# Kernel optimization log

Hardware: AMD Instinct MI355X
Metric: run time of the kernel (lower is better)

Reference implementation:

```python
import jax, jax.numpy as jnp
import numpy as np

B, T, D = 8, 4096, 512
EXPAND = 2
DI = D * EXPAND          # d_inner = 1024
K = 7                    # d_conv
LN_EPS = 1e-5


def setup_inputs() -> dict:
    key = jax.random.key(0)
    ks = jax.random.split(key, 12)
    s = 0.02
    return {
        "x": jax.random.normal(ks[0], (B, T, D), dtype=jnp.float32),
        # shared input projection (no bias): weight (2*DI, D), torch Linear layout
        "in_proj_w": jax.random.normal(ks[1], (2 * DI, D), dtype=jnp.float32) * s,
        # forward Conv1DSequenceMixer: depthwise conv (DI,1,K) + bias, proj Linear (DI,DI)+bias
        "conv_fwd_w": jax.random.normal(ks[2], (DI, 1, K), dtype=jnp.float32) * s,
        "conv_fwd_b": jnp.zeros((DI,), dtype=jnp.float32),
        "proj_fwd_w": jax.random.normal(ks[3], (DI, DI), dtype=jnp.float32) * s,
        "proj_fwd_b": jnp.zeros((DI,), dtype=jnp.float32),
        # backward Conv1DSequenceMixer
        "conv_bwd_w": jax.random.normal(ks[4], (DI, 1, K), dtype=jnp.float32) * s,
        "conv_bwd_b": jnp.zeros((DI,), dtype=jnp.float32),
        "proj_bwd_w": jax.random.normal(ks[5], (DI, DI), dtype=jnp.float32) * s,
        "proj_bwd_b": jnp.zeros((DI,), dtype=jnp.float32),
        # diagonal term and gate scale
        "diag_weight": jnp.full((DI,), 0.1, dtype=jnp.float32),
        "gate_scale": jnp.full((1,), 0.5, dtype=jnp.float32),
        # output projection (no bias): (D, DI)
        "out_proj_w": jax.random.normal(ks[6], (D, DI), dtype=jnp.float32) * s,
        # LayerNorm
        "ln_g": jnp.ones((D,), dtype=jnp.float32),
        "ln_b": jnp.zeros((D,), dtype=jnp.float32),
    }


def _seq_mixer(x, conv_w, conv_b, proj_w, proj_b):
    """Conv1DSequenceMixer: causal depthwise conv + SiLU(Linear). x: (B,T,C)."""
    C = x.shape[-1]
    # torch pads both sides by K-1 then truncates to T -> equivalent to causal left-pad
    xp = jnp.pad(x, ((0, 0), (K - 1, 0), (0, 0)))            # (B, T+K-1, C)
    y = jax.lax.conv_general_dilated(
        xp.transpose(0, 2, 1), conv_w, window_strides=(1,), padding="VALID",
        dimension_numbers=("NCH", "OIH", "NCH"), feature_group_count=C,
    )                                                         # (B, C, T)
    y = y.transpose(0, 2, 1) + conv_b                         # (B, T, C)
    y = jnp.einsum("btc,oc->bto", y, proj_w) + proj_b
    return jax.nn.silu(y)


def _shift_right(x):
    """Shift one step right along time, zero-padding the first step."""
    return jnp.pad(x, ((0, 0), (1, 0), (0, 0)))[:, :-1, :]


def reference(x, in_proj_w, conv_fwd_w, conv_fwd_b, proj_fwd_w, proj_fwd_b,
              conv_bwd_w, conv_bwd_b, proj_bwd_w, proj_bwd_b,
              diag_weight, gate_scale, out_proj_w, ln_g, ln_b):
    residual = x
    xz = jnp.einsum("btd,ed->bte", x, in_proj_w)              # (B,T,2*DI)
    x_proj, z = xz[..., :DI], xz[..., DI:]

    y_fwd = _shift_right(_seq_mixer(x_proj, conv_fwd_w, conv_fwd_b, proj_fwd_w, proj_fwd_b))

    x_flip = jnp.flip(x_proj, axis=1)
    y_bwd = _shift_right(_seq_mixer(x_flip, conv_bwd_w, conv_bwd_b, proj_bwd_w, proj_bwd_b))
    y_bwd = jnp.flip(y_bwd, axis=1)

    y = y_fwd + y_bwd + x_proj * diag_weight                  # quasiseparable sum
    y = y * jax.nn.silu(z) * gate_scale                       # SiLU gate + scale
    y = jnp.einsum("bte,de->btd", y, out_proj_w)              # out_proj (no bias)

    h = residual + y                                          # dropout=0 (eval)
    mu = jnp.mean(h, axis=-1, keepdims=True)
    var = jnp.var(h, axis=-1, keepdims=True)
    return (h - mu) * jax.lax.rsqrt(var + LN_EPS) * ln_g + ln_b
```

## Files before the change

kernel.cpp:

```cpp
#include <hip/hip_runtime.h>
#include <hip/hip_bf16.h>
#include <cstdint>

#define T_SEQ  4096
#define DMODEL 512
#define DINNER 1024
#define MTOT   32768

typedef __bf16 bf16_t;
typedef bf16_t bf16x8 __attribute__((ext_vector_type(8)));
typedef bf16_t bf16x4v __attribute__((ext_vector_type(4)));
typedef float  f32x4  __attribute__((ext_vector_type(4)));

__device__ __forceinline__ void async_copy16(const bf16_t* g, bf16_t* l) {
  __builtin_amdgcn_global_load_lds(
      (const __attribute__((address_space(1))) void*)g,
      (__attribute__((address_space(3))) void*)l,
      16, 0, 0);
}

__device__ __forceinline__ float silu_f(float v) {
  return v / (1.f + __expf(-v));
}

__device__ __forceinline__ int xcd_swizzle_flat() {
  const int nwg = gridDim.x * gridDim.y;
  const int orig = blockIdx.y * gridDim.x + blockIdx.x;
  const int q = nwg >> 3, r = nwg & 7;
  const int xcd = orig & 7, lid = orig >> 3;
  return (xcd < r ? xcd * (q + 1) : r * (q + 1) + (xcd - r) * q) + lid;
}

__global__ __launch_bounds__(256) void cast_kernel(
    const float* __restrict__ s, bf16_t* __restrict__ d, int n4)
{
  const int i = blockIdx.x * 256 + threadIdx.x;
  if (i < n4) {
    const f32x4 v = ((const f32x4*)s)[i];
    bf16x4v o;
    o[0] = (bf16_t)v[0]; o[1] = (bf16_t)v[1];
    o[2] = (bf16_t)v[2]; o[3] = (bf16_t)v[3];
    ((bf16x4v*)d)[i] = o;
  }
}

__global__ __launch_bounds__(256) void wtr_kernel(
    const float* __restrict__ w, float* __restrict__ wt)
{
  const int i = blockIdx.x * 256 + threadIdx.x;
  if (i < 7 * DINNER) {
    const int c = i & (DINNER - 1);
    const int k = i >> 10;
    wt[i] = w[c * 7 + k];
  }
}

template <int EPI>
__global__ __launch_bounds__(256, 2) void gemm_bt(
    const bf16_t* __restrict__ A, const bf16_t* __restrict__ B,
    bf16_t* __restrict__ Cb, float* __restrict__ Cf,
    const float* __restrict__ resid,
    int N, int K)
{
  constexpr int BM = 128, BN = 128, BK = 64;
  __shared__ __attribute__((aligned(16))) bf16_t sA0[BM * BK];
  __shared__ __attribute__((aligned(16))) bf16_t sB0[BN * BK];
  __shared__ __attribute__((aligned(16))) bf16_t sA1[BM * BK];
  __shared__ __attribute__((aligned(16))) bf16_t sB1[BN * BK];

  const int tid  = threadIdx.x;
  const int bflat = xcd_swizzle_flat();
  const int m0 = (bflat / gridDim.x) * BM;
  const int n0 = (bflat % gridDim.x) * BN;

  const int w    = tid >> 6, lane = tid & 63;
  const int wm   = (w & 1) << 6, wn = (w >> 1) << 6;
  const int quad = lane >> 4, lrow = lane & 15;

  const int f0 = tid << 3;
  const int sr = f0 >> 6, sc = f0 & 63;

  f32x4 acc[4][4] = {};

  auto STAGE = [&](int kt, bf16_t* dA, bf16_t* dB) {
#pragma unroll
    for (int i = 0; i < 4; ++i) {
      const int f = f0 + (i << 11);
      const int r = sr + (i << 5);
      async_copy16(&A[(size_t)(m0 + r) * K + kt + sc], &dA[f]);
      async_copy16(&B[(size_t)(n0 + r) * K + kt + sc], &dB[f]);
    }
  };

  auto COMPUTE = [&](const bf16_t* cA, const bf16_t* cB) {
#pragma unroll
    for (int ks = 0; ks < 2; ++ks) {
      const int ko = ks * 32 + (quad << 3);
      bf16x8 av[4], bv[4];
#pragma unroll
      for (int i = 0; i < 4; ++i) {
        av[i] = *(const bf16x8*)&cA[(wm + i * 16 + lrow) * BK + ko];
        bv[i] = *(const bf16x8*)&cB[(wn + i * 16 + lrow) * BK + ko];
      }
#pragma unroll
      for (int mi = 0; mi < 4; ++mi)
#pragma unroll
        for (int ni = 0; ni < 4; ++ni)
          acc[mi][ni] = __builtin_amdgcn_mfma_f32_16x16x32_bf16(
              av[mi], bv[ni], acc[mi][ni], 0, 0, 0);
    }
  };

  STAGE(0, sA0, sB0);
  __syncthreads();

  for (int kt = 0; kt < K; kt += 2 * BK) {
    if (kt + BK < K) STAGE(kt + BK, sA1, sB1);
    COMPUTE(sA0, sB0);
    __syncthreads();
    if (kt + 2 * BK < K) STAGE(kt + 2 * BK, sA0, sB0);
    COMPUTE(sA1, sB1);
    __syncthreads();
  }

#pragma unroll
  for (int mi = 0; mi < 4; ++mi)
#pragma unroll
    for (int ni = 0; ni < 4; ++ni)
#pragma unroll
      for (int r = 0; r < 4; ++r) {
        const int row = m0 + wm + mi * 16 + (quad << 2) + r;
        const int col = n0 + wn + ni * 16 + lrow;
        float v = acc[mi][ni][r];
        if constexpr (EPI == 0) {
          Cb[(size_t)row * N + col] = (bf16_t)v;
        } else {
          v += resid[(size_t)row * N + col];
          Cf[(size_t)row * N + col] = v;
        }
      }
}

__global__ __launch_bounds__(256, 2) void gemm_dual(
    const bf16_t* __restrict__ A1, const bf16_t* __restrict__ A2,
    const bf16_t* __restrict__ B1, const bf16_t* __restrict__ B2,
    const float* __restrict__ b1, const float* __restrict__ b2,
    const bf16_t* __restrict__ xzc, const float* __restrict__ diag,
    const float* __restrict__ gs, bf16_t* __restrict__ G,
    int r0, int loc0, int N, int K)
{
  constexpr int BM = 128, BN = 128, BK = 64;
  __shared__ __attribute__((aligned(16))) bf16_t sA1[BM * BK];
  __shared__ __attribute__((aligned(16))) bf16_t sA2[BM * BK];
  __shared__ __attribute__((aligned(16))) bf16_t sB1[BN * BK];
  __shared__ __attribute__((aligned(16))) bf16_t sB2[BN * BK];

  const int tid  = threadIdx.x;
  const int bflat = xcd_swizzle_flat();
  const int m0 = (bflat / gridDim.x) * BM;
  const int n0 = (bflat % gridDim.x) * BN;

  const int w    = tid >> 6, lane = tid & 63;
  const int wm   = (w & 1) << 6, wn = (w >> 1) << 6;
  const int quad = lane >> 4, lrow = lane & 15;

  f32x4 accf[4][4] = {};
  f32x4 accb[4][4] = {};

  for (int kt = 0; kt < K; kt += BK) {
    __syncthreads();
#pragma unroll
    for (int i = 0; i < 4; ++i) {
      const int f = (i * 256 + tid) << 3;
      const int r = f >> 6, c = f & 63;
      const size_t ga = (size_t)(m0 + r) * K + kt + c;
      const size_t gb = (size_t)(n0 + r) * K + kt + c;
      async_copy16(&A1[ga], &sA1[f]);
      async_copy16(&A2[ga], &sA2[f]);
      async_copy16(&B1[gb], &sB1[f]);
      async_copy16(&B2[gb], &sB2[f]);
    }
    __syncthreads();
#pragma unroll
    for (int ks = 0; ks < 2; ++ks) {
      const int ko = ks * 32 + (quad << 3);
      bf16x8 av[4], bv[4];
#pragma unroll
      for (int i = 0; i < 4; ++i) {
        av[i] = *(const bf16x8*)&sA1[(wm + i * 16 + lrow) * BK + ko];
        bv[i] = *(const bf16x8*)&sB1[(wn + i * 16 + lrow) * BK + ko];
      }
#pragma unroll
      for (int mi = 0; mi < 4; ++mi)
#pragma unroll
        for (int ni = 0; ni < 4; ++ni)
          accf[mi][ni] = __builtin_amdgcn_mfma_f32_16x16x32_bf16(
              av[mi], bv[ni], accf[mi][ni], 0, 0, 0);
#pragma unroll
      for (int i = 0; i < 4; ++i) {
        av[i] = *(const bf16x8*)&sA2[(wm + i * 16 + lrow) * BK + ko];
        bv[i] = *(const bf16x8*)&sB2[(wn + i * 16 + lrow) * BK + ko];
      }
#pragma unroll
      for (int mi = 0; mi < 4; ++mi)
#pragma unroll
        for (int ni = 0; ni < 4; ++ni)
          accb[mi][ni] = __builtin_amdgcn_mfma_f32_16x16x32_bf16(
              av[mi], bv[ni], accb[mi][ni], 0, 0, 0);
    }
  }

  const float gsv = gs[0];
  int   colv[4];
  float b1v[4], b2v[4], dgv[4];
#pragma unroll
  for (int ni = 0; ni < 4; ++ni) {
    const int col = n0 + wn + ni * 16 + lrow;
    colv[ni] = col;
    b1v[ni] = b1[col];
    b2v[ni] = b2[col];
    dgv[ni] = diag[col];
  }
#pragma unroll
  for (int mi = 0; mi < 4; ++mi)
#pragma unroll
    for (int r = 0; r < 4; ++r) {
      const int row = m0 + wm + mi * 16 + (quad << 2) + r;
      const int t = (row + r0) & (T_SEQ - 1);
      const bool tf = (t > 0), tb = (t < T_SEQ - 1);
      const bf16_t* xrow = &xzc[(size_t)(loc0 + row) * 2048];
#pragma unroll
      for (int ni = 0; ni < 4; ++ni) {
        const float sf = silu_f(accf[mi][ni][r] + b1v[ni]);
        const float sb = silu_f(accb[mi][ni][r] + b2v[ni]);
        const float xp = (float)xrow[colv[ni]];
        const float z  = (float)xrow[colv[ni] + DINNER];
        float y = xp * dgv[ni];
        if (tf) y += sf;
        if (tb) y += sb;
        G[(size_t)row * N + colv[ni]] = (bf16_t)(y * silu_f(z) * gsv);
      }
    }
}

template <int DIR>
__global__ __launch_bounds__(256) void conv_kernel(
    const bf16_t* __restrict__ xzc,
    const float* __restrict__ wt, const float* __restrict__ bc,
    bf16_t* __restrict__ vout, int r0, int loc0, int Mc)
{
  const int idx = blockIdx.x * 256 + threadIdx.x;
  const int c8  = idx & 127;
  const int tg  = idx >> 7;
  const int bt0 = tg << 2;
  const int t0  = (bt0 + r0) & (T_SEQ - 1);
  const int lt0 = bt0 + loc0;
  const int cc  = c8 << 3;

  float wv[7][8];
#pragma unroll
  for (int k = 0; k < 7; ++k) {
    const f32x4 a = *(const f32x4*)&wt[k * DINNER + cc];
    const f32x4 b = *(const f32x4*)&wt[k * DINNER + cc + 4];
#pragma unroll
    for (int u = 0; u < 4; ++u) { wv[k][u] = a[u]; wv[k][u + 4] = b[u]; }
  }

  float acc[4][8];
  {
    const f32x4 a = *(const f32x4*)&bc[cc];
    const f32x4 b = *(const f32x4*)&bc[cc + 4];
#pragma unroll
    for (int i = 0; i < 4; ++i)
#pragma unroll
      for (int u = 0; u < 4; ++u) { acc[i][u] = a[u]; acc[i][u + 4] = b[u]; }
  }

#pragma unroll
  for (int rr = 0; rr < 10; ++rr) {
    int lt = (DIR == 0) ? (lt0 - 7 + rr) : (lt0 + 1 + rr);
    lt = lt < 0 ? 0 : (lt > Mc - 1 ? Mc - 1 : lt);
    const bf16x8 xv = *(const bf16x8*)&xzc[(size_t)lt * 2048 + cc];
    float xf[8];
#pragma unroll
    for (int u = 0; u < 8; ++u) xf[u] = (float)xv[u];
#pragma unroll
    for (int i = 0; i < 4; ++i) {
      const int k = (DIR == 0) ? (rr - i) : (i + 6 - rr);
      if (k >= 0 && k <= 6) {
        const bool ok = (DIR == 0) ? (t0 + i >= 7 - k)
                                   : (t0 + i <= (T_SEQ - 8) + k);
        if (ok) {
#pragma unroll
          for (int u = 0; u < 8; ++u) acc[i][u] += wv[k][u] * xf[u];
        }
      }
    }
  }

#pragma unroll
  for (int i = 0; i < 4; ++i) {
    bf16x8 o;
#pragma unroll
    for (int u = 0; u < 8; ++u) o[u] = (bf16_t)acc[i][u];
    *(bf16x8*)&vout[(size_t)(bt0 + i) * DINNER + cc] = o;
  }
}

__global__ __launch_bounds__(256) void ln_kernel(
    const float* __restrict__ h,
    const float* __restrict__ lng, const float* __restrict__ lnb,
    float* __restrict__ out, int r0)
{
  const int row = blockIdx.x;
  const int tid = threadIdx.x;
  const float* hr = h + (size_t)row * DMODEL;
  const float v0 = hr[tid], v1 = hr[tid + 256];
  float s  = v0 + v1;
  float ss = v0 * v0 + v1 * v1;
#pragma unroll
  for (int off = 1; off < 64; off <<= 1) {
    s  += __shfl_xor(s, off);
    ss += __shfl_xor(ss, off);
  }
  __shared__ float ps[8];
  const int w = tid >> 6;
  if ((tid & 63) == 0) { ps[w] = s; ps[w + 4] = ss; }
  __syncthreads();
  s  = ps[0] + ps[1] + ps[2] + ps[3];
  ss = ps[4] + ps[5] + ps[6] + ps[7];
  const float mu  = s * (1.f / DMODEL);
  const float inv = rsqrtf(ss * (1.f / DMODEL) - mu * mu + 1e-5f);
  float* o = out + (size_t)(r0 + row) * DMODEL;
  o[tid]       = (v0 - mu) * inv * lng[tid]       + lnb[tid];
  o[tid + 256] = (v1 - mu) * inv * lng[tid + 256] + lnb[tid + 256];
}

extern "C" void kernel_launch(void* const* d_in, const int* in_sizes, int n_in,
                              void* d_out, int out_size, void* d_ws, size_t ws_size,
                              hipStream_t stream) {
  const float* x    = (const float*)d_in[0];
  const float* in_w = (const float*)d_in[1];
  const float* cfw  = (const float*)d_in[2];
  const float* cfb  = (const float*)d_in[3];
  const float* pfw  = (const float*)d_in[4];
  const float* pfb  = (const float*)d_in[5];
  const float* cbw  = (const float*)d_in[6];
  const float* cbb  = (const float*)d_in[7];
  const float* pbw  = (const float*)d_in[8];
  const float* pbb  = (const float*)d_in[9];
  const float* diag = (const float*)d_in[10];
  const float* gs   = (const float*)d_in[11];
  const float* ow   = (const float*)d_in[12];
  const float* lng  = (const float*)d_in[13];
  const float* lnb  = (const float*)d_in[14];
  float* out = (float*)d_out;

  char* ws = (char*)d_ws;

  bf16_t* xw   = (bf16_t*)(ws);
  bf16_t* inwb = (bf16_t*)(ws + (size_t)33554432);
  bf16_t* pfwb = (bf16_t*)(ws + (size_t)35651584);
  bf16_t* pbwb = (bf16_t*)(ws + (size_t)37748736);
  bf16_t* owb  = (bf16_t*)(ws + (size_t)39845888);
  float*  wtf  = (float*)(ws + (size_t)40894464);
  float*  wtb  = (float*)(ws + (size_t)40923136);
  const size_t persist = 40951808;

  int CH = 128;
  {
    const int cands[9] = {32768, 16384, 8192, 4096, 2048, 1024, 512, 256, 128};
    for (int i = 0; i < 9; ++i) {
      const size_t req = persist + (size_t)(cands[i] + 256) * 4096 +
                         (size_t)3 * cands[i] * 2048;
      if (ws_size >= req) { CH = cands[i]; break; }
    }
  }

  char* cb = ws + persist;
  const size_t xz_cap = (size_t)(CH + 256) * 4096;
  bf16_t* xzc  = (bf16_t*)cb;
  bf16_t* bufA = (bf16_t*)(cb + xz_cap);
  bf16_t* bufB = (bf16_t*)(cb + xz_cap + (size_t)CH * 2048);
  bf16_t* bufC = (bf16_t*)(cb + xz_cap + (size_t)CH * 4096);
  float*  hbuf = (float*)cb;

  dim3 blk(256);

  cast_kernel<<<dim3(16384), blk, 0, stream>>>(x,    xw,   4194304);
  cast_kernel<<<dim3(1024),  blk, 0, stream>>>(in_w, inwb, 262144);
  cast_kernel<<<dim3(1024),  blk, 0, stream>>>(pfw,  pfwb, 262144);
  cast_kernel<<<dim3(1024),  blk, 0, stream>>>(pbw,  pbwb, 262144);
  cast_kernel<<<dim3(512),   blk, 0, stream>>>(ow,   owb,  131072);
  wtr_kernel<<<dim3(28), blk, 0, stream>>>(cfw, wtf);
  wtr_kernel<<<dim3(28), blk, 0, stream>>>(cbw, wtb);

  for (int r0 = 0; r0 < MTOT; r0 += CH) {
    const int g0 = (r0 >= 128) ? (r0 - 128) : 0;
    int g1 = r0 + CH + 128; if (g1 > MTOT) g1 = MTOT;
    const int Mc   = g1 - g0;
    const int loc0 = r0 - g0;

    gemm_bt<0><<<dim3(2048 / 128, Mc / 128), blk, 0, stream>>>(
        xw + (size_t)g0 * 512, inwb, xzc, nullptr, nullptr, 2048, 512);

    conv_kernel<0><<<dim3(CH / 8), blk, 0, stream>>>(
        xzc, wtf, cfb, bufA, r0, loc0, Mc);

    conv_kernel<1><<<dim3(CH / 8), blk, 0, stream>>>(
        xzc, wtb, cbb, bufB, r0, loc0, Mc);

    gemm_dual<<<dim3(1024 / 128, CH / 128), blk, 0, stream>>>(
        bufA, bufB, pfwb, pbwb, pfb, pbb, xzc, diag, gs, bufC,
        r0, loc0, 1024, 1024);

    gemm_bt<2><<<dim3(512 / 128, CH / 128), blk, 0, stream>>>(
        bufC, owb, nullptr, hbuf, x + (size_t)r0 * 512, 512, 1024);

    ln_kernel<<<dim3(CH), blk, 0, stream>>>(hbuf, lng, lnb, out, r0);
  }
}
```

Baseline: 641.8 us.

## Software-pipeline dual GEMM by overlapping loads of one operand pair with compute of other

The dual GEMM loop used to load all four tiles and then compute both products, with barriers that left loads and MFMA serialized. It now stages the A2/B2 tiles while computing with A1/B1, then prefetches the next A1/B1 tiles while computing with A2/B2, so async global-to-LDS copies overlap with MFMA work. The number of barriers per k-step stays the same, and correctness depends on the async copies being complete by each barrier.

```diff
diff --git a/kernel.cpp b/kernel.cpp
--- a/kernel.cpp
+++ b/kernel.cpp
@@ -150,10 +150,10 @@
     int r0, int loc0, int N, int K)
 {
   constexpr int BM = 128, BN = 128, BK = 64;
-  __shared__ __attribute__((aligned(16))) bf16_t sA1[BM * BK];
-  __shared__ __attribute__((aligned(16))) bf16_t sA2[BM * BK];
-  __shared__ __attribute__((aligned(16))) bf16_t sB1[BN * BK];
-  __shared__ __attribute__((aligned(16))) bf16_t sB2[BN * BK];
+  __shared__ __attribute__((aligned(16))) bf16_t sA1l[BM * BK];
+  __shared__ __attribute__((aligned(16))) bf16_t sA2l[BM * BK];
+  __shared__ __attribute__((aligned(16))) bf16_t sB1l[BN * BK];
+  __shared__ __attribute__((aligned(16))) bf16_t sB2l[BN * BK];
 
   const int tid  = threadIdx.x;
   const int bflat = xcd_swizzle_flat();
@@ -164,50 +164,52 @@
   const int wm   = (w & 1) << 6, wn = (w >> 1) << 6;
   const int quad = lane >> 4, lrow = lane & 15;
 
+  const int f0 = tid << 3;
+  const int sr = f0 >> 6, sc = f0 & 63;
+
   f32x4 accf[4][4] = {};
   f32x4 accb[4][4] = {};
 
-  for (int kt = 0; kt < K; kt += BK) {
-    __syncthreads();
+  auto STAGE = [&](int kt, const bf16_t* gA, const bf16_t* gB,
+                   bf16_t* dA, bf16_t* dB) {
 #pragma unroll
     for (int i = 0; i < 4; ++i) {
-      const int f = (i * 256 + tid) << 3;
-      const int r = f >> 6, c = f & 63;
-      const size_t ga = (size_t)(m0 + r) * K + kt + c;
-      const size_t gb = (size_t)(n0 + r) * K + kt + c;
-      async_copy16(&A1[ga], &sA1[f]);
-      async_copy16(&A2[ga], &sA2[f]);
-      async_copy16(&B1[gb], &sB1[f]);
-      async_copy16(&B2[gb], &sB2[f]);
-    }
-    __syncthreads();
+      const int f = f0 + (i << 11);
+      const int r = sr + (i << 5);
+      async_copy16(&gA[(size_t)(m0 + r) * K + kt + sc], &dA[f]);
+      async_copy16(&gB[(size_t)(n0 + r) * K + kt + sc], &dB[f]);
+    }
+  };
+
+  auto COMPUTE = [&](const bf16_t* cA, const bf16_t* cB, f32x4 (*acc)[4]) {
 #pragma unroll
     for (int ks = 0; ks < 2; ++ks) {
       const int ko = ks * 32 + (quad << 3);
       bf16x8 av[4], bv[4];
 #pragma unroll
       for (int i = 0; i < 4; ++i) {
-        av[i] = *(const bf16x8*)&sA1[(wm + i * 16 + lrow) * BK + ko];
-        bv[i] = *(const bf16x8*)&sB1[(wn + i * 16 + lrow) * BK + ko];
+        av[i] = *(const bf16x8*)&cA[(wm + i * 16 + lrow) * BK + ko];
+        bv[i] = *(const bf16x8*)&cB[(wn + i * 16 + lrow) * BK + ko];
       }
 #pragma unroll
       for (int mi = 0; mi < 4; ++mi)
 #pragma unroll
         for (int ni = 0; ni < 4; ++ni)
-          accf[mi][ni] = __builtin_amdgcn_mfma_f32_16x16x32_bf16(
-              av[mi], bv[ni], accf[mi][ni], 0, 0, 0);
-#pragma unroll
-      for (int i = 0; i < 4; ++i) {
-        av[i] = *(const bf16x8*)&sA2[(wm + i * 16 + lrow) * BK + ko];
-        bv[i] = *(const bf16x8*)&sB2[(wn + i * 16 + lrow) * BK + ko];
-      }
-#pragma unroll
-      for (int mi = 0; mi < 4; ++mi)
-#pragma unroll
-        for (int ni = 0; ni < 4; ++ni)
-          accb[mi][ni] = __builtin_amdgcn_mfma_f32_16x16x32_bf16(
-              av[mi], bv[ni], accb[mi][ni], 0, 0, 0);
-    }
+          acc[mi][ni] = __builtin_amdgcn_mfma_f32_16x16x32_bf16(
+              av[mi], bv[ni], acc[mi][ni], 0, 0, 0);
+    }
+  };
+
+  STAGE(0, A1, B1, sA1l, sB1l);
+  __syncthreads();
+
+  for (int kt = 0; kt < K; kt += BK) {
+    STAGE(kt, A2, B2, sA2l, sB2l);
+    COMPUTE(sA1l, sB1l, accf);
+    __syncthreads();
+    if (kt + BK < K) STAGE(kt + BK, A1, B1, sA1l, sB1l);
+    COMPUTE(sA2l, sB2l, accb);
+    __syncthreads();
   }
 
   const float gsv = gs[0];
```

After: 621.9 us. 3.1% less time.
